# Performance work log

Hardware: AMD Instinct MI355X
Metric: run time of the kernel (lower is better)

## Reference

```python
import jax, jax.numpy as jnp
import numpy as np

IN_CH, OUT_CH, K, STRIDE, PAD = 256, 256, 5, 1, 2


def setup_inputs() -> dict:
    key = jax.random.key(0)
    kx, kw = jax.random.split(key)
    x = jax.random.normal(kx, (32, IN_CH, 4096), dtype=jnp.float32)
    # kaiming_uniform_(a=sqrt(5)) -> bound = 1/sqrt(fan_in), fan_in = in_ch*k
    bound = 1.0 / np.sqrt(IN_CH * K)
    weight = jax.random.uniform(kw, (OUT_CH, IN_CH, K), dtype=jnp.float32,
                                minval=-bound, maxval=bound)
    bias = jnp.zeros((OUT_CH,), dtype=jnp.float32)
    return {"x": x, "weight": weight, "bias": bias}


def reference(x, weight, bias):
    # x: [B, C_in, W]; weight: [C_out, C_in, K] -> out: [B, C_out, W_out]
    out = jax.lax.conv_general_dilated(
        x, weight,
        window_strides=(STRIDE,),
        padding=[(PAD, PAD)],
        dimension_numbers=("NCH", "OIH", "NCH"),
    )
    return out + bias[None, :, None]
```

## Files before the change

kernel.cpp:

```cpp
#include <hip/hip_runtime.h>
#include <hip/hip_bf16.h>

typedef unsigned short u16;
typedef unsigned int u32;
typedef __attribute__((ext_vector_type(8))) short short8;
typedef __attribute__((ext_vector_type(4))) float floatx4;

#define NB 32
#define NCI 256
#define NCO 256
#define NW 4096
#define NK 5

#define WSTEP 16384
#define W2_BYTES (40 * WSTEP)

#define XROWB 64
#define XROWS 260
#define XBUF (XROWS * XROWB)
#define XSWZ(r) ((((r) >> 1) & 3) << 4)

#define FENCE asm volatile("" ::: "memory")
#define LK0   asm volatile("s_waitcnt lgkmcnt(0)" ::: "memory")
#define VM0   asm volatile("s_waitcnt vmcnt(0)" ::: "memory")


__global__ void wprep(const float* __restrict__ wgt, u16* __restrict__ W2) {
    int i = blockIdx.x * 256 + threadIdx.x;
    if (i >= NCO * NCI * NK) return;
    int k  = i % NK;
    int ci = (i / NK) % NCI;
    int co = i / (NCI * NK);
    int cb = ci >> 5, cr = ci & 31;
    int s    = cb * NK + k;
    int slot = (cr >> 3) ^ ((co >> 1) & 3);
    __hip_bfloat16 h = __float2bfloat16(wgt[i]);
    W2[(size_t)(s * 256 + co) * 32 + slot * 8 + (cr & 7)] = *reinterpret_cast<u16*>(&h);
}

__device__ __forceinline__ u16 bf16bits(float f) {
    __hip_bfloat16 h = __float2bfloat16(f);
    return *reinterpret_cast<u16*>(&h);
}

__device__ __forceinline__ void gload_lds16(const void* gsrc, void* ldst) {
    __builtin_amdgcn_global_load_lds(
        (const __attribute__((address_space(1))) unsigned int*)gsrc,
        (__attribute__((address_space(3))) unsigned int*)ldst, 16, 0, 0);
}


__global__ __launch_bounds__(512, 2)
void conv_mfma(const float* __restrict__ x, const u16* __restrict__ W2,
               const float* __restrict__ bias, float* __restrict__ out) {
    __shared__ __align__(16) char smem[2 * WSTEP + 2 * XBUF];
    char* const wlds = smem;
    char* const xlds = smem + 2 * WSTEP;

    const int bid  = blockIdx.x;
    const int wt   = bid & 15;
    const int b    = bid >> 4;
    const int tid  = threadIdx.x;
    const int lane = tid & 63;
    const int wave = tid >> 6;
    const int wm   = wave >> 2;
    const int wn   = wave & 3;
    const int mrow = lane & 15;
    const int g    = lane >> 4;
    const int w0   = wt * 256;

    floatx4 acc[8][4];
#pragma unroll
    for (int mi = 0; mi < 8; ++mi)
#pragma unroll
        for (int ni = 0; ni < 4; ++ni)
            acc[mi][ni] = (floatx4){0.f, 0.f, 0.f, 0.f};

    const float* xb   = x + (size_t)b * NCI * NW;
    const char*  wimg = (const char*)W2;

    const int wloc = tid & 255;
    const int h    = tid >> 8;
    const int soff0 = (2 + wloc) * XROWB + ((h * 32) ^ XSWZ(2 + wloc));
    const int soff1 = (2 + wloc) * XROWB + ((h * 32 + 16) ^ XSWZ(2 + wloc));
    const float* xcol = xb + w0 + wloc;

    const int hidx = wave * 16 + (lane & 15);
    const int hri  = hidx >> 5;
    const int hci  = hidx & 31;
    const int hwg  = (hri < 2) ? (w0 - 2 + hri) : (w0 + 256 + (hri - 2));
    const int hwc  = (hwg < 0) ? 0 : ((hwg > NW - 1) ? (NW - 1) : hwg);
    const bool hok = (hwg >= 0) && (hwg < NW);
    const int hrloc = (hri < 2) ? hri : (258 + (hri - 2));
    const int hoff  = hrloc * XROWB + (((hci >> 3) ^ ((hrloc >> 1) & 3)) * 16) + (hci & 7) * 2;

    float v[16];
    float hvv = 0.f;

    {
        gload_lds16(wimg + (wave * 2) * 1024 + lane * 16, wlds + (wave * 2) * 1024);
        gload_lds16(wimg + (wave * 2 + 1) * 1024 + lane * 16, wlds + (wave * 2 + 1) * 1024);
        float v0[16];
#pragma unroll
        for (int j = 0; j < 16; ++j)
            v0[j] = xcol[(size_t)(h * 16 + j) * NW];
        float hv0 = xb[(size_t)hci * NW + hwc];
        u32 p[8];
#pragma unroll
        for (int jp = 0; jp < 8; ++jp)
            p[jp] = (u32)bf16bits(v0[2 * jp]) | ((u32)bf16bits(v0[2 * jp + 1]) << 16);
        *(int4*)(xlds + soff0) = *(int4*)&p[0];
        *(int4*)(xlds + soff1) = *(int4*)&p[4];
        if ((lane & 63) < 16)
            *(u16*)(xlds + hoff) = bf16bits(hok ? hv0 : 0.f);
        LK0; VM0;
#pragma unroll
        for (int j = 0; j < 16; ++j)
            v[j] = xcol[(size_t)(32 + h * 16 + j) * NW];
        hvv = xb[(size_t)(32 + hci) * NW + hwc];
    }
    FENCE; __builtin_amdgcn_s_barrier(); FENCE;

    for (int cb = 0; cb < 8; ++cb) {
        const char* xcur = xlds + (cb & 1) * XBUF;
        char* xnxt       = xlds + ((cb + 1) & 1) * XBUF;
#pragma unroll
        for (int t = 0; t < NK; ++t) {
            const int s = cb * NK + t;
            if (s < 39) {
                const char* src = wimg + (size_t)(s + 1) * WSTEP;
                char* dst = wlds + ((s + 1) & 1) * WSTEP;
                gload_lds16(src + (wave * 2) * 1024 + lane * 16, dst + (wave * 2) * 1024);
                gload_lds16(src + (wave * 2 + 1) * 1024 + lane * 16, dst + (wave * 2 + 1) * 1024);
            }
            FENCE;
            const char* wcur = wlds + (s & 1) * WSTEP;
            short8 af[8], bf[4];
#pragma unroll
            for (int mi = 0; mi < 8; ++mi) {
                int rw = wm * 128 + mi * 16 + mrow;
                af[mi] = *(const short8*)(wcur + rw * 64 + ((g * 16) ^ XSWZ(rw)));
            }
#pragma unroll
            for (int ni = 0; ni < 4; ++ni) {
                int rx = wn * 64 + ni * 16 + mrow + t;
                bf[ni] = *(const short8*)(xcur + rx * XROWB + ((g * 16) ^ XSWZ(rx)));
            }
            __builtin_amdgcn_s_setprio(1);
#pragma unroll
            for (int mi = 0; mi < 8; ++mi)
#pragma unroll
                for (int ni = 0; ni < 4; ++ni)
                    acc[mi][ni] = __builtin_amdgcn_mfma_f32_16x16x32_bf16(
                        af[mi], bf[ni], acc[mi][ni], 0, 0, 0);
            __builtin_amdgcn_s_setprio(0);

            if (t == 4) {
                if (cb < 7) {
                    u32 p[8];
#pragma unroll
                    for (int jp = 0; jp < 8; ++jp)
                        p[jp] = (u32)bf16bits(v[2 * jp]) | ((u32)bf16bits(v[2 * jp + 1]) << 16);
                    *(int4*)(xnxt + soff0) = *(int4*)&p[0];
                    *(int4*)(xnxt + soff1) = *(int4*)&p[4];
                    if ((lane & 63) < 16)
                        *(u16*)(xnxt + hoff) = bf16bits(hok ? hvv : 0.f);
                    LK0; VM0;
                    if (cb < 6) {
                        const float* sx = xcol + (size_t)((cb + 2) * 32 + h * 16) * NW;
                        FENCE;
#pragma unroll
                        for (int j = 0; j < 16; ++j)
                            v[j] = sx[(size_t)j * NW];
                        hvv = xb[(size_t)((cb + 2) * 32 + hci) * NW + hwc];
                    }
                    FENCE; __builtin_amdgcn_s_barrier(); FENCE;
                }
            } else {
                VM0;
                FENCE; __builtin_amdgcn_s_barrier(); FENCE;
            }
        }
    }

#pragma unroll
    for (int mi = 0; mi < 8; ++mi) {
        int cobase = wm * 128 + mi * 16 + g * 4;
        float bv[4];
#pragma unroll
        for (int r = 0; r < 4; ++r) bv[r] = bias[cobase + r];
#pragma unroll
        for (int ni = 0; ni < 4; ++ni) {
            int col = w0 + wn * 64 + ni * 16 + mrow;
#pragma unroll
            for (int r = 0; r < 4; ++r)
                out[((size_t)b * NCO + cobase + r) * NW + col] =
                    acc[mi][ni][r] + bv[r];
        }
    }
}


__global__ void conv_naive(const float* __restrict__ x, const float* __restrict__ wgt,
                           const float* __restrict__ bias, float* __restrict__ out) {
    int w  = blockIdx.x * 256 + threadIdx.x;
    int co = blockIdx.y;
    int b  = blockIdx.z;
    float acc = bias[co];
    for (int ci = 0; ci < NCI; ci++) {
        const float* xr = x + ((size_t)b * NCI + ci) * NW;
        const float* wr = wgt + ((size_t)co * NCI + ci) * NK;
#pragma unroll
        for (int k = 0; k < NK; k++) {
            int wi = w + k - 2;
            if (wi >= 0 && wi < NW) acc += xr[wi] * wr[k];
        }
    }
    out[((size_t)b * NCO + co) * NW + w] = acc;
}


extern "C" void kernel_launch(void* const* d_in, const int* in_sizes, int n_in,
                              void* d_out, int out_size, void* d_ws, size_t ws_size,
                              hipStream_t stream) {
    const float* x    = (const float*)d_in[0];
    const float* wgt  = (const float*)d_in[1];
    const float* bias = (const float*)d_in[2];
    float* out        = (float*)d_out;

    if (ws_size < (size_t)W2_BYTES) {
        conv_naive<<<dim3(NW / 256, NCO, NB), 256, 0, stream>>>(x, wgt, bias, out);
        return;
    }

    u16* W2 = (u16*)d_ws;
    wprep<<<(NCO * NCI * NK + 255) / 256, 256, 0, stream>>>(wgt, W2);
    conv_mfma<<<512, 512, 0, stream>>>(x, W2, bias, out);
}
```

Measured before the change: 105.8 us.

## Group weight taps into two-stage LDS chunks to halve barriers per channel block

Weight staging now loads up to two filter taps (32 KB) per pipeline stage, splitting each 5-tap channel block into groups of 2,2,1. This cuts the per-block barrier and wait count from five to three. The x prefetch for the next channel block moves to the start of the block instead of being issued a block ahead, and the outer loop is fully unrolled. LDS use grows by 32 KB, which may limit occupancy at two blocks per CU. The shorter x prefetch distance may also expose global load latency.

```diff
diff --git a/kernel.cpp b/kernel.cpp
--- a/kernel.cpp
+++ b/kernel.cpp
@@ -14,6 +14,7 @@
 
 #define WSTEP 16384
 #define W2_BYTES (40 * WSTEP)
+#define WREG 32768
 
 #define XROWB 64
 #define XROWS 260
@@ -53,9 +54,9 @@
 __global__ __launch_bounds__(512, 2)
 void conv_mfma(const float* __restrict__ x, const u16* __restrict__ W2,
                const float* __restrict__ bias, float* __restrict__ out) {
-    __shared__ __align__(16) char smem[2 * WSTEP + 2 * XBUF];
+    __shared__ __align__(16) char smem[2 * WREG + 2 * XBUF];
     char* const wlds = smem;
-    char* const xlds = smem + 2 * WSTEP;
+    char* const xlds = smem + 2 * WREG;
 
     const int bid  = blockIdx.x;
     const int wt   = bid & 15;
@@ -98,8 +99,11 @@
     float hvv = 0.f;
 
     {
-        gload_lds16(wimg + (wave * 2) * 1024 + lane * 16, wlds + (wave * 2) * 1024);
-        gload_lds16(wimg + (wave * 2 + 1) * 1024 + lane * 16, wlds + (wave * 2 + 1) * 1024);
+#pragma unroll
+        for (int k = 0; k < 4; ++k) {
+            int c = wave + 8 * k;
+            gload_lds16(wimg + c * 1024 + lane * 16, wlds + c * 1024);
+        }
         float v0[16];
 #pragma unroll
         for (int j = 0; j < 16; ++j)
@@ -114,70 +118,77 @@
         if ((lane & 63) < 16)
             *(u16*)(xlds + hoff) = bf16bits(hok ? hv0 : 0.f);
         LK0; VM0;
-#pragma unroll
-        for (int j = 0; j < 16; ++j)
-            v[j] = xcol[(size_t)(32 + h * 16 + j) * NW];
-        hvv = xb[(size_t)(32 + hci) * NW + hwc];
     }
     FENCE; __builtin_amdgcn_s_barrier(); FENCE;
 
+#pragma unroll
     for (int cb = 0; cb < 8; ++cb) {
         const char* xcur = xlds + (cb & 1) * XBUF;
         char* xnxt       = xlds + ((cb + 1) & 1) * XBUF;
 #pragma unroll
-        for (int t = 0; t < NK; ++t) {
-            const int s = cb * NK + t;
-            if (s < 39) {
-                const char* src = wimg + (size_t)(s + 1) * WSTEP;
-                char* dst = wlds + ((s + 1) & 1) * WSTEP;
-                gload_lds16(src + (wave * 2) * 1024 + lane * 16, dst + (wave * 2) * 1024);
-                gload_lds16(src + (wave * 2 + 1) * 1024 + lane * 16, dst + (wave * 2 + 1) * 1024);
+        for (int j = 0; j < 3; ++j) {
+            const int gr = cb * 3 + j;
+            const int fs = cb * 5 + (j == 0 ? 0 : (j == 1 ? 2 : 4));
+            const int nt = (j == 2) ? 1 : 2;
+
+            if (gr < 23) {
+                const int cbn = (gr + 1) / 3, jn = (gr + 1) % 3;
+                const int fsn = cbn * 5 + (jn == 0 ? 0 : (jn == 1 ? 2 : 4));
+                const int ntn = (jn == 2) ? 1 : 2;
+                const char* src = wimg + (size_t)fsn * WSTEP;
+                char* dst = wlds + ((gr + 1) & 1) * WREG;
+#pragma unroll
+                for (int k = 0; k < 2 * ntn; ++k) {
+                    int c = wave + 8 * k;
+                    gload_lds16(src + c * 1024 + lane * 16, dst + c * 1024);
+                }
             }
             FENCE;
-            const char* wcur = wlds + (s & 1) * WSTEP;
-            short8 af[8], bf[4];
-#pragma unroll
-            for (int mi = 0; mi < 8; ++mi) {
-                int rw = wm * 128 + mi * 16 + mrow;
-                af[mi] = *(const short8*)(wcur + rw * 64 + ((g * 16) ^ XSWZ(rw)));
-            }
-#pragma unroll
-            for (int ni = 0; ni < 4; ++ni) {
-                int rx = wn * 64 + ni * 16 + mrow + t;
-                bf[ni] = *(const short8*)(xcur + rx * XROWB + ((g * 16) ^ XSWZ(rx)));
-            }
-            __builtin_amdgcn_s_setprio(1);
-#pragma unroll
-            for (int mi = 0; mi < 8; ++mi)
-#pragma unroll
-                for (int ni = 0; ni < 4; ++ni)
-                    acc[mi][ni] = __builtin_amdgcn_mfma_f32_16x16x32_bf16(
-                        af[mi], bf[ni], acc[mi][ni], 0, 0, 0);
-            __builtin_amdgcn_s_setprio(0);
-
-            if (t == 4) {
-                if (cb < 7) {
-                    u32 p[8];
-#pragma unroll
-                    for (int jp = 0; jp < 8; ++jp)
-                        p[jp] = (u32)bf16bits(v[2 * jp]) | ((u32)bf16bits(v[2 * jp + 1]) << 16);
-                    *(int4*)(xnxt + soff0) = *(int4*)&p[0];
-                    *(int4*)(xnxt + soff1) = *(int4*)&p[4];
-                    if ((lane & 63) < 16)
-                        *(u16*)(xnxt + hoff) = bf16bits(hok ? hvv : 0.f);
-                    LK0; VM0;
-                    if (cb < 6) {
-                        const float* sx = xcol + (size_t)((cb + 2) * 32 + h * 16) * NW;
-                        FENCE;
-#pragma unroll
-                        for (int j = 0; j < 16; ++j)
-                            v[j] = sx[(size_t)j * NW];
-                        hvv = xb[(size_t)((cb + 2) * 32 + hci) * NW + hwc];
-                    }
-                    FENCE; __builtin_amdgcn_s_barrier(); FENCE;
+            if (j == 0 && cb < 7) {
+                const float* sx = xcol + (size_t)((cb + 1) * 32 + h * 16) * NW;
+#pragma unroll
+                for (int jj = 0; jj < 16; ++jj)
+                    v[jj] = sx[(size_t)jj * NW];
+                hvv = xb[(size_t)((cb + 1) * 32 + hci) * NW + hwc];
+            }
+            FENCE;
+#pragma unroll
+            for (int tt = 0; tt < nt; ++tt) {
+                const int s = fs + tt;
+                const int t = s - cb * 5;
+                const char* wcur = wlds + (gr & 1) * WREG + tt * WSTEP;
+                short8 af[8], bf[4];
+#pragma unroll
+                for (int mi = 0; mi < 8; ++mi) {
+                    int rw = wm * 128 + mi * 16 + mrow;
+                    af[mi] = *(const short8*)(wcur + rw * 64 + ((g * 16) ^ XSWZ(rw)));
                 }
-            } else {
-                VM0;
+#pragma unroll
+                for (int ni = 0; ni < 4; ++ni) {
+                    int rx = wn * 64 + ni * 16 + mrow + t;
+                    bf[ni] = *(const short8*)(xcur + rx * XROWB + ((g * 16) ^ XSWZ(rx)));
+                }
+                __builtin_amdgcn_s_setprio(1);
+#pragma unroll
+                for (int mi = 0; mi < 8; ++mi)
+#pragma unroll
+                    for (int ni = 0; ni < 4; ++ni)
+                        acc[mi][ni] = __builtin_amdgcn_mfma_f32_16x16x32_bf16(
+                            af[mi], bf[ni], acc[mi][ni], 0, 0, 0);
+                __builtin_amdgcn_s_setprio(0);
+            }
+            if (j == 2 && cb < 7) {
+                u32 p[8];
+#pragma unroll
+                for (int jp = 0; jp < 8; ++jp)
+                    p[jp] = (u32)bf16bits(v[2 * jp]) | ((u32)bf16bits(v[2 * jp + 1]) << 16);
+                *(int4*)(xnxt + soff0) = *(int4*)&p[0];
+                *(int4*)(xnxt + soff1) = *(int4*)&p[4];
+                if ((lane & 63) < 16)
+                    *(u16*)(xnxt + hoff) = bf16bits(hok ? hvv : 0.f);
+            }
+            if (gr < 23) {
+                LK0; VM0;
                 FENCE; __builtin_amdgcn_s_barrier(); FENCE;
             }
         }
```

New measurement: 141.6 us. +33.8%, slower.
